# Kernel tuning notes

Measured on AMD Instinct MI355X. Metric: run time of the kernel, lower is better.

The kernel has to match this reference:

```python
import jax, jax.numpy as jnp
import numpy as np

N = 100000
E = 1600000
D_IN = 128
D_OUT = 128
HEADS = 4
C = D_OUT // HEADS  # per-head channels = 32
NEG_SLOPE = 0.2
EPS_SOFTMAX = 1e-16
EPS_LN = 1e-5


def setup_inputs() -> dict:
    key = jax.random.key(0)
    ks = jax.random.split(key, 10)
    x = jax.random.normal(ks[0], (N, D_IN), dtype=jnp.float32)
    edge_index = jax.random.randint(ks[1], (2, E), 0, N, dtype=jnp.int64)
    s = 1.0 / np.sqrt(D_IN)
    W = jax.random.normal(ks[2], (D_IN, HEADS * C), dtype=jnp.float32) * s
    att_src = jax.random.normal(ks[3], (HEADS, C), dtype=jnp.float32) * (1.0 / np.sqrt(C))
    att_dst = jax.random.normal(ks[4], (HEADS, C), dtype=jnp.float32) * (1.0 / np.sqrt(C))
    gat_bias = jax.random.normal(ks[5], (D_OUT,), dtype=jnp.float32) * 0.02
    skip_W = jax.random.normal(ks[6], (D_IN, D_OUT), dtype=jnp.float32) * s
    skip_b = jax.random.normal(ks[7], (D_OUT,), dtype=jnp.float32) * 0.02
    ln_g = jnp.ones((D_OUT,), dtype=jnp.float32)
    ln_b = jnp.zeros((D_OUT,), dtype=jnp.float32)
    return {"x": x, "edge_index": edge_index, "W": W, "att_src": att_src,
            "att_dst": att_dst, "gat_bias": gat_bias, "skip_W": skip_W,
            "skip_b": skip_b, "ln_g": ln_g, "ln_b": ln_b}


def _gat_edge_conv(x, src, dst, W, att_src, att_dst, gat_bias, skip_W, skip_b, ln_g, ln_b):
    n = x.shape[0]
    h = (x @ W).reshape(n, HEADS, C)                      # [N,H,C]
    a_s = jnp.einsum('nhc,hc->nh', h, att_src)            # [N,H]
    a_d = jnp.einsum('nhc,hc->nh', h, att_dst)            # [N,H]
    e = jax.nn.leaky_relu(a_s[src] + a_d[dst], NEG_SLOPE)  # [E,H]
    # segment softmax over incoming edges of each dst node
    m = jax.ops.segment_max(e, dst, num_segments=n)        # [N,H]
    p = jnp.exp(e - m[dst])
    z = jax.ops.segment_sum(p, dst, num_segments=n)        # [N,H]
    alpha = p / (z[dst] + EPS_SOFTMAX)                     # [E,H]
    msg = h[src] * alpha[:, :, None]                       # [E,H,C]
    out = jax.ops.segment_sum(msg, dst, num_segments=n)    # [N,H,C]
    out = out.reshape(n, HEADS * C) + gat_bias
    out = out + x @ skip_W + skip_b
    mu = out.mean(-1, keepdims=True)
    var = ((out - mu) ** 2).mean(-1, keepdims=True)
    return (out - mu) * jax.lax.rsqrt(var + EPS_LN) * ln_g + ln_b


def reference(x, edge_index, W, att_src, att_dst, gat_bias, skip_W, skip_b, ln_g, ln_b):
    n = x.shape[0]
    loops = jnp.arange(n, dtype=edge_index.dtype)          # PyG GATConv add_self_loops=True
    src = jnp.concatenate([edge_index[0], loops])
    dst = jnp.concatenate([edge_index[1], loops])
    return _gat_edge_conv(x, src, dst, W, att_src, att_dst, gat_bias, skip_W, skip_b, ln_g, ln_b)
```

## Files before the change

kernel.cpp:

```cpp
#include <hip/hip_runtime.h>
#include <hip/hip_bf16.h>

#define D 128
#define HEADS 4
#define NEG_SLOPE 0.2f
#define QSCALE 0.0625f
#define QUNSCALE 16.0f

typedef __attribute__((ext_vector_type(8))) short short8;
typedef __attribute__((ext_vector_type(4))) float f32x4;
typedef __attribute__((ext_vector_type(2))) _Float16 h2;

__device__ __forceinline__ float lrelu(float v) {
    return fmaxf(v, NEG_SLOPE * v);
}

__device__ __forceinline__ short f2bf(float v) {
    __hip_bfloat16 b = __float2bfloat16(v);
    short s;
    __builtin_memcpy(&s, &b, 2);
    return s;
}

__device__ __forceinline__ unsigned short f2h(float v) {
    _Float16 h = (_Float16)v;
    unsigned short s;
    __builtin_memcpy(&s, &h, 2);
    return s;
}

#define BCAP 4608
__global__ __launch_bounds__(256)
void wprep_kernel(const float* __restrict__ W, const float* __restrict__ S,
                  short* __restrict__ wsT, int* __restrict__ woffA, int nb) {
    int idx = blockIdx.x * 256 + threadIdx.x;
    int nn = idx >> 7, k = idx & 127;
    float v = (nn < 128) ? W[k * D + nn] : S[k * D + (nn - 128)];
    wsT[idx] = f2bf(v);
    if (idx < nb) woffA[idx] = idx * BCAP;
}

#define LDSPAD 136
__global__ __launch_bounds__(512, 4)
void gemm_mfma_kernel(const float* __restrict__ x, const short* __restrict__ wsT,
                      const float* __restrict__ skip_b, const float* __restrict__ gat_bias,
                      const float* __restrict__ att_src, const float* __restrict__ att_dst,
                      unsigned short* __restrict__ hb, unsigned short* __restrict__ baseb,
                      float* __restrict__ a_s, float* __restrict__ a_d, int n) {
    __shared__ short xs[64][LDSPAD];
    const int t = threadIdx.x;
    const int row0 = blockIdx.x * 64;
    #pragma unroll
    for (int i = 0; i < 4; ++i) {
        int f = t + 512 * i;
        int row = f >> 5, c4 = (f & 31) * 4;
        float4 v = make_float4(0.f, 0.f, 0.f, 0.f);
        if (row0 + row < n) v = *(const float4*)&x[(size_t)(row0 + row) * D + c4];
        short4 s4;
        s4.x = f2bf(v.x); s4.y = f2bf(v.y); s4.z = f2bf(v.z); s4.w = f2bf(v.w);
        *(short4*)&xs[row][c4] = s4;
    }
    __syncthreads();
    const int wv = t >> 6, lane = t & 63;
    const int lo = lane & 15, hi = lane >> 4;
    const int wr = wv >> 2;
    const int wc = wv & 3;
    f32x4 acc[2][4] = {};
    #pragma unroll
    for (int k0 = 0; k0 < 128; k0 += 32) {
        const int kk = k0 + hi * 8;
        short8 a0 = *(const short8*)&xs[wr * 32 + lo][kk];
        short8 a1 = *(const short8*)&xs[wr * 32 + 16 + lo][kk];
        #pragma unroll
        for (int nt = 0; nt < 4; ++nt) {
            short8 b = *(const short8*)&wsT[(wc * 64 + nt * 16 + lo) * D + kk];
            acc[0][nt] = __builtin_amdgcn_mfma_f32_16x16x32_bf16(a0, b, acc[0][nt], 0, 0, 0);
            acc[1][nt] = __builtin_amdgcn_mfma_f32_16x16x32_bf16(a1, b, acc[1][nt], 0, 0, 0);
        }
    }
    if (wc < 2) {
        float as_[4], ad_[4];
        #pragma unroll
        for (int nt = 0; nt < 4; ++nt) {
            const int c = wc * 64 + nt * 16 + lo;
            as_[nt] = att_src[c];
            ad_[nt] = att_dst[c];
        }
        #pragma unroll
        for (int mt = 0; mt < 2; ++mt) {
            #pragma unroll
            for (int reg = 0; reg < 4; ++reg) {
                float ps0 = acc[mt][0][reg] * as_[0] + acc[mt][1][reg] * as_[1];
                float ps1 = acc[mt][2][reg] * as_[2] + acc[mt][3][reg] * as_[3];
                float pd0 = acc[mt][0][reg] * ad_[0] + acc[mt][1][reg] * ad_[1];
                float pd1 = acc[mt][2][reg] * ad_[2] + acc[mt][3][reg] * ad_[3];
                #pragma unroll
                for (int off = 1; off < 16; off <<= 1) {
                    ps0 += __shfl_xor(ps0, off, 64);
                    ps1 += __shfl_xor(ps1, off, 64);
                    pd0 += __shfl_xor(pd0, off, 64);
                    pd1 += __shfl_xor(pd1, off, 64);
                }
                if (lo == 0) {
                    const int r = row0 + wr * 32 + mt * 16 + hi * 4 + reg;
                    if (r < n) {
                        a_s[r * HEADS + wc * 2 + 0] = ps0;
                        a_s[r * HEADS + wc * 2 + 1] = ps1;
                        a_d[r * HEADS + wc * 2 + 0] = pd0;
                        a_d[r * HEADS + wc * 2 + 1] = pd1;
                    }
                }
            }
        }
    }
    #pragma unroll
    for (int nt = 0; nt < 4; ++nt) {
        const int cc = wc * 64 + nt * 16 + lo;
        const bool isH = cc < 128;
        const float bb = isH ? 0.f : (skip_b[cc - 128] + gat_bias[cc - 128]);
        unsigned short* dst = isH ? hb : baseb;
        const int c = isH ? cc : cc - 128;
        #pragma unroll
        for (int mt = 0; mt < 2; ++mt) {
            const int rbase = row0 + wr * 32 + mt * 16 + hi * 4;
            #pragma unroll
            for (int reg = 0; reg < 4; ++reg) {
                const int r = rbase + reg;
                if (r < n) dst[(size_t)r * D + c] = f2h(acc[mt][nt][reg] + bb);
            }
        }
    }
}

#define BEPT 16
#define BCHUNK (256 * BEPT)

__global__ __launch_bounds__(256)
void binA_kernel(const int* __restrict__ ei, int* __restrict__ woffA,
                 unsigned int* __restrict__ pairs, int E_, int nb) {
    __shared__ int hist[512];
    __shared__ int gbase[512];
    const int t = threadIdx.x;
    for (int q = t; q < 512; q += 256) hist[q] = 0;
    __syncthreads();
    int sv[BEPT], dv[BEPT], rk[BEPT];
    const int base = blockIdx.x * BCHUNK;
    #pragma unroll
    for (int i = 0; i < BEPT; ++i) {
        int e = base + i * 256 + t;
        if (e < E_) {
            sv[i] = ei[e];
            dv[i] = ei[E_ + e];
            rk[i] = atomicAdd(&hist[dv[i] >> 8], 1);
        } else {
            sv[i] = -1;
        }
    }
    __syncthreads();
    for (int q = t; q < nb; q += 256) {
        int v = hist[q];
        gbase[q] = v ? atomicAdd(&woffA[q], v) : 0;
    }
    __syncthreads();
    #pragma unroll
    for (int i = 0; i < BEPT; ++i) {
        if (sv[i] >= 0) {
            int pos = gbase[dv[i] >> 8] + rk[i];
            pairs[pos] = ((unsigned int)sv[i] << 8) | (unsigned int)(dv[i] & 255);
        }
    }
}

#define KCAP 24
__global__ __launch_bounds__(256)
void binB_kernel(const unsigned int* __restrict__ pairs, const int* __restrict__ wcur,
                 int* __restrict__ cnt, int* __restrict__ offs,
                 int* __restrict__ ssrc, int n) {
    __shared__ int nhist[256];
    __shared__ int sc[256];
    __shared__ int nbase[256];
    const int b = blockIdx.x;
    const int t = threadIdx.x;
    const int node0 = b << 8;
    const int sbeg = b * BCAP, send = wcur[b];
    nhist[t] = 0;
    __syncthreads();
    unsigned int pk[KCAP];
    int rk[KCAP];
    int nl = 0;
    for (int e = sbeg + t; e < send; e += 256) {
        unsigned int p = pairs[e];
        int r = atomicAdd(&nhist[p & 255], 1);
        if (nl < KCAP) { pk[nl] = p; rk[nl] = r; }
        ++nl;
    }
    __syncthreads();
    int v = nhist[t];
    sc[t] = v;
    __syncthreads();
    for (int off = 1; off < 256; off <<= 1) {
        int x = (t >= off) ? sc[t - off] : 0;
        __syncthreads();
        sc[t] += x;
        __syncthreads();
    }
    int ex = sc[t] - v;
    nbase[t] = sbeg + ex;
    if (node0 + t < n) {
        cnt[node0 + t] = v;
        offs[node0 + t] = sbeg + ex;
    }
    __syncthreads();
    const int m = nl < KCAP ? nl : KCAP;
    for (int i = 0; i < m; ++i) {
        int pos = nbase[pk[i] & 255] + rk[i];
        ssrc[pos] = (int)(pk[i] >> 8);
    }
}

__global__ __launch_bounds__(256)
void gather_kernel(const int* __restrict__ offs, const int* __restrict__ cnt,
                   const int* __restrict__ ssrc, const float* __restrict__ a_s,
                   const float* __restrict__ a_d, const uint2* __restrict__ hb4,
                   const uint2* __restrict__ baseb4,
                   const float* __restrict__ ln_g, const float* __restrict__ ln_b,
                   float* __restrict__ out, int n) {
    const int lane = threadIdx.x & 63;
    const int i = blockIdx.x * 4 + (threadIdx.x >> 6);
    if (i >= n) return;
    const int e4 = lane >> 2, h4 = lane & 3;
    const int l31 = lane & 31;
    const int myhead = l31 >> 3;
    const int esel = (lane < 32) ? 0 : 1;
    const uint2 bv = baseb4[(size_t)i * 32 + l31];
    const float4 g4 = ((const float4*)ln_g)[l31];
    const float4 lb4 = ((const float4*)ln_b)[l31];
    const float as_h4 = a_s[i * HEADS + h4];
    const float ad_h4 = a_d[i * HEADS + h4];
    const float qself = __expf(lrelu(as_h4 + ad_h4));
    float zacc = (e4 == 0) ? qself : 0.f;
    h2 acc01, acc23;
    {
        uint2 u = hb4[(size_t)i * 32 + l31];
        float qs = __shfl(qself, myhead, 64) * QSCALE;
        float w = (lane < 32) ? qs : 0.f;
        const _Float16 wh = (_Float16)w;
        const h2 w2 = {wh, wh};
        acc01 = __builtin_bit_cast(h2, u.x) * w2;
        acc23 = __builtin_bit_cast(h2, u.y) * w2;
    }
    const int o = offs[i];
    const int c = cnt[i];
    for (int k0 = 0; k0 < c; k0 += 16) {
        const int rem = c - k0;
        int srow = 0;
        float q = 0.f;
        if (e4 < rem) {
            const int sidx = ssrc[o + k0 + e4];
            srow = sidx << 5;
            q = __expf(lrelu(a_s[sidx * HEADS + h4] + ad_h4));
        }
        zacc += q;
        const _Float16 qh = (_Float16)(q * QSCALE);
        const h2 qv = {qh, qh};
        const int qpk = __builtin_bit_cast(int, qv);
        const int m = rem < 16 ? rem : 16;
        int ee = 0;
        for (; ee + 8 <= m; ee += 8) {
            const int sl0 = (ee + 0 + esel) * 4;
            const int sl1 = (ee + 2 + esel) * 4;
            const int sl2 = (ee + 4 + esel) * 4;
            const int sl3 = (ee + 6 + esel) * 4;
            const int rA = __shfl(srow, sl0, 64) + l31;
            const int rB = __shfl(srow, sl1, 64) + l31;
            const int rC = __shfl(srow, sl2, 64) + l31;
            const int rD = __shfl(srow, sl3, 64) + l31;
            const h2 qA = __builtin_bit_cast(h2, __shfl(qpk, sl0 + myhead, 64));
            const h2 qB = __builtin_bit_cast(h2, __shfl(qpk, sl1 + myhead, 64));
            const h2 qC = __builtin_bit_cast(h2, __shfl(qpk, sl2 + myhead, 64));
            const h2 qD = __builtin_bit_cast(h2, __shfl(qpk, sl3 + myhead, 64));
            const uint2 uA = hb4[(size_t)(unsigned)rA];
            const uint2 uB = hb4[(size_t)(unsigned)rB];
            const uint2 uC = hb4[(size_t)(unsigned)rC];
            const uint2 uD = hb4[(size_t)(unsigned)rD];
            acc01 += __builtin_bit_cast(h2, uA.x) * qA;
            acc23 += __builtin_bit_cast(h2, uA.y) * qA;
            acc01 += __builtin_bit_cast(h2, uB.x) * qB;
            acc23 += __builtin_bit_cast(h2, uB.y) * qB;
            acc01 += __builtin_bit_cast(h2, uC.x) * qC;
            acc23 += __builtin_bit_cast(h2, uC.y) * qC;
            acc01 += __builtin_bit_cast(h2, uD.x) * qD;
            acc23 += __builtin_bit_cast(h2, uD.y) * qD;
        }
        for (; ee < m; ee += 2) {
            const int sl = (ee + esel) * 4;
            const int rA = __shfl(srow, sl, 64) + l31;
            const h2 qA = __builtin_bit_cast(h2, __shfl(qpk, sl + myhead, 64));
            const uint2 uA = hb4[(size_t)(unsigned)rA];
            acc01 += __builtin_bit_cast(h2, uA.x) * qA;
            acc23 += __builtin_bit_cast(h2, uA.y) * qA;
        }
    }
    float acc0 = (float)acc01.x;
    float acc1 = (float)acc01.y;
    float acc2 = (float)acc23.x;
    float acc3 = (float)acc23.y;
    acc0 += __shfl_xor(acc0, 32, 64);
    acc1 += __shfl_xor(acc1, 32, 64);
    acc2 += __shfl_xor(acc2, 32, 64);
    acc3 += __shfl_xor(acc3, 32, 64);
    #pragma unroll
    for (int off = 4; off < 64; off <<= 1) zacc += __shfl_xor(zacc, off, 64);
    const float zz = __shfl(zacc, myhead, 64);
    const float rz = QUNSCALE / (zz + 1e-16f);
    const h2 b01 = __builtin_bit_cast(h2, bv.x);
    const h2 b23 = __builtin_bit_cast(h2, bv.y);
    float v0 = acc0 * rz + (float)b01.x;
    float v1 = acc1 * rz + (float)b01.y;
    float v2 = acc2 * rz + (float)b23.x;
    float v3 = acc3 * rz + (float)b23.y;
    float s1 = v0 + v1 + v2 + v3;
    float s2 = v0 * v0 + v1 * v1 + v2 * v2 + v3 * v3;
    #pragma unroll
    for (int off = 1; off < 32; off <<= 1) {
        s1 += __shfl_xor(s1, off, 64);
        s2 += __shfl_xor(s2, off, 64);
    }
    const float mu = s1 * (1.f / 128.f);
    const float var = s2 * (1.f / 128.f) - mu * mu;
    const float r = rsqrtf(var + 1e-5f);
    if (lane < 32) {
        float4 o4;
        o4.x = (v0 - mu) * r * g4.x + lb4.x;
        o4.y = (v1 - mu) * r * g4.y + lb4.y;
        o4.z = (v2 - mu) * r * g4.z + lb4.z;
        o4.w = (v3 - mu) * r * g4.w + lb4.w;
        ((float4*)out)[(size_t)i * 32 + l31] = o4;
    }
}

extern "C" void kernel_launch(void* const* d_in, const int* in_sizes, int n_in,
                              void* d_out, int out_size, void* d_ws, size_t ws_size,
                              hipStream_t stream) {
    const float* x        = (const float*)d_in[0];
    const int*   ei       = (const int*)d_in[1];
    const float* W        = (const float*)d_in[2];
    const float* att_src  = (const float*)d_in[3];
    const float* att_dst  = (const float*)d_in[4];
    const float* gat_bias = (const float*)d_in[5];
    const float* skip_W   = (const float*)d_in[6];
    const float* skip_b   = (const float*)d_in[7];
    const float* ln_g     = (const float*)d_in[8];
    const float* ln_b     = (const float*)d_in[9];
    float* out = (float*)d_out;

    const int n  = in_sizes[0] / D;
    const int E_ = in_sizes[1] / 2;
    const int nb = (n + 255) >> 8;

    char* p = (char*)d_ws;
    auto carve = [&p](size_t bytes) {
        char* r = p;
        p += (bytes + 255) & ~(size_t)255;
        return r;
    };
    short* wsT            = (short*)carve(32768 * sizeof(short));
    unsigned short* hb    = (unsigned short*)carve((size_t)n * D * 2);
    unsigned short* baseb = (unsigned short*)carve((size_t)n * D * 2);
    float* a_s            = (float*)carve((size_t)n * HEADS * 4);
    float* a_d            = (float*)carve((size_t)n * HEADS * 4);
    int*   cnt            = (int*)carve((size_t)n * 4);
    int*   offs           = (int*)carve((size_t)n * 4);
    int*   woffA          = (int*)carve(512 * 4);
    int*   ssrc           = (int*)carve((size_t)nb * BCAP * 4);
    unsigned int* pairs   = (unsigned int*)carve((size_t)nb * BCAP * 4);

    wprep_kernel<<<128, 256, 0, stream>>>(W, skip_W, wsT, woffA, nb);
    gemm_mfma_kernel<<<(n + 63) / 64, 512, 0, stream>>>(x, wsT, skip_b, gat_bias,
                                                        att_src, att_dst,
                                                        hb, baseb, a_s, a_d, n);
    const int BA = (E_ + BCHUNK - 1) / BCHUNK;
    binA_kernel<<<BA, 256, 0, stream>>>(ei, woffA, pairs, E_, nb);
    binB_kernel<<<nb, 256, 0, stream>>>(pairs, woffA, cnt, offs, ssrc, n);
    gather_kernel<<<(n + 3) / 4, 256, 0, stream>>>(offs, cnt, ssrc, a_s, a_d,
                                                   (const uint2*)hb,
                                                   (const uint2*)baseb,
                                                   ln_g, ln_b, out, n);
}
```

Measured before the change: 283.6 us.

## Gather 16-byte feature rows with four edges per wave iteration

The gather kernel now has each lane load 16 bytes (8 fp16 features) of a neighbor row, so 16 lanes cover one 128-feature row and a wave processes four edges at a time instead of two. The partial sums across the four lane groups are combined with fp16 shuffle reductions, and the output is written as float2 nontemporal stores. This is meant to halve the number of gather load instructions and shuffles per edge. The cost is more accumulator registers, a wider cross-group reduction in fp16 (a possible precision change), and tail edges now run with lanes masked off.

```diff
diff --git a/kernel.cpp b/kernel.cpp
--- a/kernel.cpp
+++ b/kernel.cpp
@@ -9,6 +9,7 @@
 
 typedef __attribute__((ext_vector_type(8))) short short8;
 typedef __attribute__((ext_vector_type(4))) float f32x4;
+typedef __attribute__((ext_vector_type(2))) float f32x2;
 typedef __attribute__((ext_vector_type(2))) _Float16 h2;
 
 __device__ __forceinline__ float lrelu(float v) {
@@ -221,33 +222,36 @@
 __global__ __launch_bounds__(256)
 void gather_kernel(const int* __restrict__ offs, const int* __restrict__ cnt,
                    const int* __restrict__ ssrc, const float* __restrict__ a_s,
-                   const float* __restrict__ a_d, const uint2* __restrict__ hb4,
-                   const uint2* __restrict__ baseb4,
+                   const float* __restrict__ a_d, const uint4* __restrict__ hb16,
+                   const uint4* __restrict__ baseb16,
                    const float* __restrict__ ln_g, const float* __restrict__ ln_b,
                    float* __restrict__ out, int n) {
     const int lane = threadIdx.x & 63;
     const int i = blockIdx.x * 4 + (threadIdx.x >> 6);
     if (i >= n) return;
     const int e4 = lane >> 2, h4 = lane & 3;
-    const int l31 = lane & 31;
-    const int myhead = l31 >> 3;
-    const int esel = (lane < 32) ? 0 : 1;
-    const uint2 bv = baseb4[(size_t)i * 32 + l31];
-    const float4 g4 = ((const float4*)ln_g)[l31];
-    const float4 lb4 = ((const float4*)ln_b)[l31];
+    const int l15 = lane & 15;
+    const int grp = lane >> 4;
+    const int hh = l15 >> 2;
+    const uint4 bv = baseb16[(size_t)i * 16 + l15];
+    const float2 g2 = ((const float2*)ln_g)[l15 * 4 + grp];
+    const float2 lb2 = ((const float2*)ln_b)[l15 * 4 + grp];
     const float as_h4 = a_s[i * HEADS + h4];
     const float ad_h4 = a_d[i * HEADS + h4];
     const float qself = __expf(lrelu(as_h4 + ad_h4));
     float zacc = (e4 == 0) ? qself : 0.f;
-    h2 acc01, acc23;
+    h2 acc0 = {0.f, 0.f}, acc1 = {0.f, 0.f}, acc2 = {0.f, 0.f}, acc3 = {0.f, 0.f};
     {
-        uint2 u = hb4[(size_t)i * 32 + l31];
-        float qs = __shfl(qself, myhead, 64) * QSCALE;
-        float w = (lane < 32) ? qs : 0.f;
-        const _Float16 wh = (_Float16)w;
-        const h2 w2 = {wh, wh};
-        acc01 = __builtin_bit_cast(h2, u.x) * w2;
-        acc23 = __builtin_bit_cast(h2, u.y) * w2;
+        const float qs = __shfl(qself, hh, 64) * QSCALE;
+        if (grp == 0) {
+            const uint4 u = hb16[(size_t)i * 16 + l15];
+            const _Float16 wh = (_Float16)qs;
+            const h2 w2 = {wh, wh};
+            acc0 = __builtin_bit_cast(h2, u.x) * w2;
+            acc1 = __builtin_bit_cast(h2, u.y) * w2;
+            acc2 = __builtin_bit_cast(h2, u.z) * w2;
+            acc3 = __builtin_bit_cast(h2, u.w) * w2;
+        }
     }
     const int o = offs[i];
     const int c = cnt[i];
@@ -257,7 +261,7 @@
         float q = 0.f;
         if (e4 < rem) {
             const int sidx = ssrc[o + k0 + e4];
-            srow = sidx << 5;
+            srow = sidx << 4;
             q = __expf(lrelu(a_s[sidx * HEADS + h4] + ad_h4));
         }
         zacc += q;
@@ -267,76 +271,77 @@
         const int m = rem < 16 ? rem : 16;
         int ee = 0;
         for (; ee + 8 <= m; ee += 8) {
-            const int sl0 = (ee + 0 + esel) * 4;
-            const int sl1 = (ee + 2 + esel) * 4;
-            const int sl2 = (ee + 4 + esel) * 4;
-            const int sl3 = (ee + 6 + esel) * 4;
-            const int rA = __shfl(srow, sl0, 64) + l31;
-            const int rB = __shfl(srow, sl1, 64) + l31;
-            const int rC = __shfl(srow, sl2, 64) + l31;
-            const int rD = __shfl(srow, sl3, 64) + l31;
-            const h2 qA = __builtin_bit_cast(h2, __shfl(qpk, sl0 + myhead, 64));
-            const h2 qB = __builtin_bit_cast(h2, __shfl(qpk, sl1 + myhead, 64));
-            const h2 qC = __builtin_bit_cast(h2, __shfl(qpk, sl2 + myhead, 64));
-            const h2 qD = __builtin_bit_cast(h2, __shfl(qpk, sl3 + myhead, 64));
-            const uint2 uA = hb4[(size_t)(unsigned)rA];
-            const uint2 uB = hb4[(size_t)(unsigned)rB];
-            const uint2 uC = hb4[(size_t)(unsigned)rC];
-            const uint2 uD = hb4[(size_t)(unsigned)rD];
-            acc01 += __builtin_bit_cast(h2, uA.x) * qA;
-            acc23 += __builtin_bit_cast(h2, uA.y) * qA;
-            acc01 += __builtin_bit_cast(h2, uB.x) * qB;
-            acc23 += __builtin_bit_cast(h2, uB.y) * qB;
-            acc01 += __builtin_bit_cast(h2, uC.x) * qC;
-            acc23 += __builtin_bit_cast(h2, uC.y) * qC;
-            acc01 += __builtin_bit_cast(h2, uD.x) * qD;
-            acc23 += __builtin_bit_cast(h2, uD.y) * qD;
-        }
-        for (; ee < m; ee += 2) {
-            const int sl = (ee + esel) * 4;
-            const int rA = __shfl(srow, sl, 64) + l31;
-            const h2 qA = __builtin_bit_cast(h2, __shfl(qpk, sl + myhead, 64));
-            const uint2 uA = hb4[(size_t)(unsigned)rA];
-            acc01 += __builtin_bit_cast(h2, uA.x) * qA;
-            acc23 += __builtin_bit_cast(h2, uA.y) * qA;
-        }
-    }
-    float acc0 = (float)acc01.x;
-    float acc1 = (float)acc01.y;
-    float acc2 = (float)acc23.x;
-    float acc3 = (float)acc23.y;
-    acc0 += __shfl_xor(acc0, 32, 64);
-    acc1 += __shfl_xor(acc1, 32, 64);
-    acc2 += __shfl_xor(acc2, 32, 64);
-    acc3 += __shfl_xor(acc3, 32, 64);
+            const int slA = (ee + grp) << 2;
+            const int slB = (ee + 4 + grp) << 2;
+            const int rA = __shfl(srow, slA, 64) + l15;
+            const int rB = __shfl(srow, slB, 64) + l15;
+            const h2 qA = __builtin_bit_cast(h2, __shfl(qpk, slA + hh, 64));
+            const h2 qB = __builtin_bit_cast(h2, __shfl(qpk, slB + hh, 64));
+            const uint4 uA = hb16[(size_t)(unsigned)rA];
+            const uint4 uB = hb16[(size_t)(unsigned)rB];
+            acc0 += __builtin_bit_cast(h2, uA.x) * qA;
+            acc1 += __builtin_bit_cast(h2, uA.y) * qA;
+            acc2 += __builtin_bit_cast(h2, uA.z) * qA;
+            acc3 += __builtin_bit_cast(h2, uA.w) * qA;
+            acc0 += __builtin_bit_cast(h2, uB.x) * qB;
+            acc1 += __builtin_bit_cast(h2, uB.y) * qB;
+            acc2 += __builtin_bit_cast(h2, uB.z) * qB;
+            acc3 += __builtin_bit_cast(h2, uB.w) * qB;
+        }
+        for (; ee < m; ee += 4) {
+            const int slot = ee + grp;
+            const int sl = slot << 2;
+            const int rA = __shfl(srow, sl, 64) + l15;
+            const h2 qA = __builtin_bit_cast(h2, __shfl(qpk, sl + hh, 64));
+            if (slot < m) {
+                const uint4 uA = hb16[(size_t)(unsigned)rA];
+                acc0 += __builtin_bit_cast(h2, uA.x) * qA;
+                acc1 += __builtin_bit_cast(h2, uA.y) * qA;
+                acc2 += __builtin_bit_cast(h2, uA.z) * qA;
+                acc3 += __builtin_bit_cast(h2, uA.w) * qA;
+            }
+        }
+    }
+    #pragma unroll
+    for (int off = 16; off < 64; off <<= 1) {
+        acc0 += __builtin_bit_cast(h2, __shfl_xor(__builtin_bit_cast(int, acc0), off, 64));
+        acc1 += __builtin_bit_cast(h2, __shfl_xor(__builtin_bit_cast(int, acc1), off, 64));
+        acc2 += __builtin_bit_cast(h2, __shfl_xor(__builtin_bit_cast(int, acc2), off, 64));
+        acc3 += __builtin_bit_cast(h2, __shfl_xor(__builtin_bit_cast(int, acc3), off, 64));
+    }
     #pragma unroll
     for (int off = 4; off < 64; off <<= 1) zacc += __shfl_xor(zacc, off, 64);
-    const float zz = __shfl(zacc, myhead, 64);
+    const float zz = __shfl(zacc, hh, 64);
     const float rz = QUNSCALE / (zz + 1e-16f);
-    const h2 b01 = __builtin_bit_cast(h2, bv.x);
-    const h2 b23 = __builtin_bit_cast(h2, bv.y);
-    float v0 = acc0 * rz + (float)b01.x;
-    float v1 = acc1 * rz + (float)b01.y;
-    float v2 = acc2 * rz + (float)b23.x;
-    float v3 = acc3 * rz + (float)b23.y;
-    float s1 = v0 + v1 + v2 + v3;
-    float s2 = v0 * v0 + v1 * v1 + v2 * v2 + v3 * v3;
-    #pragma unroll
-    for (int off = 1; off < 32; off <<= 1) {
+    const h2 b0 = __builtin_bit_cast(h2, bv.x);
+    const h2 b1 = __builtin_bit_cast(h2, bv.y);
+    const h2 b2 = __builtin_bit_cast(h2, bv.z);
+    const h2 b3 = __builtin_bit_cast(h2, bv.w);
+    const float v0 = (float)acc0.x * rz + (float)b0.x;
+    const float v1 = (float)acc0.y * rz + (float)b0.y;
+    const float v2 = (float)acc1.x * rz + (float)b1.x;
+    const float v3 = (float)acc1.y * rz + (float)b1.y;
+    const float v4 = (float)acc2.x * rz + (float)b2.x;
+    const float v5 = (float)acc2.y * rz + (float)b2.y;
+    const float v6 = (float)acc3.x * rz + (float)b3.x;
+    const float v7 = (float)acc3.y * rz + (float)b3.y;
+    float s1 = v0 + v1 + v2 + v3 + v4 + v5 + v6 + v7;
+    float s2 = v0 * v0 + v1 * v1 + v2 * v2 + v3 * v3
+             + v4 * v4 + v5 * v5 + v6 * v6 + v7 * v7;
+    #pragma unroll
+    for (int off = 1; off < 16; off <<= 1) {
         s1 += __shfl_xor(s1, off, 64);
         s2 += __shfl_xor(s2, off, 64);
     }
     const float mu = s1 * (1.f / 128.f);
     const float var = s2 * (1.f / 128.f) - mu * mu;
     const float r = rsqrtf(var + 1e-5f);
-    if (lane < 32) {
-        float4 o4;
-        o4.x = (v0 - mu) * r * g4.x + lb4.x;
-        o4.y = (v1 - mu) * r * g4.y + lb4.y;
-        o4.z = (v2 - mu) * r * g4.z + lb4.z;
-        o4.w = (v3 - mu) * r * g4.w + lb4.w;
-        ((float4*)out)[(size_t)i * 32 + l31] = o4;
-    }
+    const float lo = grp == 0 ? v0 : grp == 1 ? v2 : grp == 2 ? v4 : v6;
+    const float hi = grp == 0 ? v1 : grp == 1 ? v3 : grp == 2 ? v5 : v7;
+    f32x2 o2;
+    o2.x = (lo - mu) * r * g2.x + lb2.x;
+    o2.y = (hi - mu) * r * g2.y + lb2.y;
+    __builtin_nontemporal_store(o2, (f32x2*)out + ((size_t)i * 64 + l15 * 4 + grp));
 }
 
 extern "C" void kernel_launch(void* const* d_in, const int* in_sizes, int n_in,
@@ -383,7 +388,7 @@
     binA_kernel<<<BA, 256, 0, stream>>>(ei, woffA, pairs, E_, nb);
     binB_kernel<<<nb, 256, 0, stream>>>(pairs, woffA, cnt, offs, ssrc, n);
     gather_kernel<<<(n + 3) / 4, 256, 0, stream>>>(offs, cnt, ssrc, a_s, a_d,
-                                                   (const uint2*)hb,
-                                                   (const uint2*)baseb,
+                                                   (const uint4*)hb,
+                                                   (const uint4*)baseb,
                                                    ln_g, ln_b, out, n);
 }
```

New measurement: 284.4 us. No clear change (+0.3%).
